# Kernel tuning notes

Measured on AMD Instinct MI355X. Metric: run time of the kernel, lower is better.

Reference implementation:

```python
import jax, jax.numpy as jnp
import numpy as np
from jax import lax

D_MODEL = 1024
N_HEADS = 16
D_STATE = 1024
D_INNER = 1024
D_CONV = 4
CHUNK = 64
BATCH = 2
SEQ = 4096
CONV_DIM = 2 * D_STATE + D_INNER  # 3072
D_IN_PROJ = CONV_DIM + N_HEADS    # 3088


def segsum(a):
    """a: [..., T] -> [..., T, T] segment-sum: out[i,j] = sum_{j<k<=i} a[k], -inf above diag."""
    T = a.shape[-1]
    idx = jnp.arange(T)
    strict = idx[:, None] > idx[None, :]          # i > j
    xx = jnp.where(strict, a[..., :, None], 0.0)  # broadcast a along new last (e) dim
    s = jnp.cumsum(xx, axis=-2)
    incl = idx[:, None] >= idx[None, :]
    return jnp.where(incl, s, -jnp.inf)


def ssd(xv, A, Bm, Cm, l):
    """Mamba-2 SSD chunked scan with max-normalized decays and norm denominator.
    xv:[b,S,h,p] A:[b,S,h] Bm:[b,S,h,n] Cm:[b,S,h,n]"""
    b, S, h, p = xv.shape
    n = Bm.shape[-1]
    c = S // l
    xv = xv.reshape(b, c, l, h, p)
    A = A.reshape(b, c, l, h)
    Bm = Bm.reshape(b, c, l, h, n)
    Cm = Cm.reshape(b, c, l, h, n)
    A = jnp.transpose(A, (0, 3, 1, 2))                  # b h c l
    A_cumsum = jnp.cumsum(A, axis=-1)                   # b h c l
    L_log = segsum(A)                                   # b h c l l
    L = jnp.exp(L_log - jnp.max(L_log, axis=-1, keepdims=True))
    norm_diag = jnp.transpose(L.sum(-1), (0, 2, 3, 1))  # b c l h
    Y_diag = jnp.einsum('bclhn,bcshn,bhcls,bcshp->bclhp', Cm, Bm, L, xv)
    decay_states = A_cumsum[..., -1:] - A_cumsum        # b h c l
    decay_states = jnp.exp(decay_states - jnp.max(decay_states, axis=-1, keepdims=True))
    norm_decay = jnp.transpose(decay_states.sum(-1), (0, 2, 1))  # b c h
    states = jnp.einsum('bclhn,bhcl,bclhp->bchpn', Bm, decay_states, xv)
    norm_decay = jnp.pad(norm_decay, ((0, 0), (1, 0), (0, 0)))
    states = jnp.pad(states, ((0, 0), (1, 0), (0, 0), (0, 0), (0, 0)))
    A_last = jnp.pad(A_cumsum[..., -1], ((0, 0), (0, 0), (1, 0)))  # b h c+1
    decay_chunk = segsum(A_last)                        # b h c+1 c+1
    decay_chunk = jnp.exp(decay_chunk - jnp.max(decay_chunk, axis=-1, keepdims=True))
    norm_decay = jnp.einsum('bhzc,bch->bzh', decay_chunk, norm_decay)[:, :-1]  # b c h
    states = jnp.einsum('bhzc,bchpn->bzhpn', decay_chunk, states)[:, :-1]      # b c h p n
    state_decay_out = jnp.exp(A_cumsum - jnp.max(A_cumsum, axis=-1, keepdims=True))
    norm_off = jnp.einsum('bch,bhcl->bclh', norm_decay, state_decay_out)
    Y_off = jnp.einsum('bclhn,bchpn,bhcl->bclhp', Cm, states, state_decay_out)
    Y = (Y_diag + Y_off).reshape(b, S, h, p)
    norm = (norm_diag + norm_off).reshape(b, S, h)
    return Y / norm[..., None]


def setup_inputs() -> dict:
    key = jax.random.key(0)
    ks = jax.random.split(key, 6)
    x = jax.random.normal(ks[0], (BATCH, SEQ, D_MODEL), dtype=jnp.float32)
    in_proj_w = jax.random.normal(ks[1], (D_IN_PROJ, D_MODEL), dtype=jnp.float32) * 0.02
    conv_w = jax.random.normal(ks[2], (CONV_DIM, 1, D_CONV), dtype=jnp.float32) * 0.3
    conv_b = jnp.zeros((CONV_DIM,), dtype=jnp.float32)
    w_base = jax.random.uniform(ks[3], (N_HEADS,), dtype=jnp.float32, minval=-0.5, maxval=0.5)
    out_proj_w = jax.random.normal(ks[4], (D_MODEL, D_INNER), dtype=jnp.float32) * 0.02
    return {"x": x, "in_proj_w": in_proj_w, "conv_w": conv_w, "conv_b": conv_b,
            "w_base": w_base, "out_proj_w": out_proj_w}


def reference(x, in_proj_w, conv_w, conv_b, w_base, out_proj_w):
    b, S, _ = x.shape  # S divisible by CHUNK -> no padding branch
    xIOw = x @ in_proj_w.T                                  # [b,S,3088]
    xIO, w = xIOw[..., :CONV_DIM], xIOw[..., CONV_DIM:]
    # causal depthwise conv1d (pad d_conv-1 on both sides, keep first S == left pad)
    y = lax.conv_general_dilated(
        jnp.transpose(xIO, (0, 2, 1)), conv_w, window_strides=(1,),
        padding=[(D_CONV - 1, 0)], feature_group_count=CONV_DIM,
        dimension_numbers=('NCH', 'OIH', 'NCH'))
    xIO = jnp.transpose(y + conv_b[None, :, None], (0, 2, 1))  # [b,S,3072]
    xs = xIO[..., :D_STATE].reshape(b, S, N_HEADS, D_STATE // N_HEADS)
    I = xIO[..., D_STATE:2 * D_STATE].reshape(b, S, N_HEADS, D_STATE // N_HEADS)
    O = xIO[..., 2 * D_STATE:].reshape(b, S, N_HEADS, D_INNER // N_HEADS)
    w = w * w_base                                          # [b,S,h]
    out = ssd(O, w, I, xs, CHUNK)                           # [b,S,h,p]
    out = out.reshape(b, S, D_INNER) @ out_proj_w.T
    return out[:, :S]
```

## Files before the change

### kernel.cpp

```cpp
#include <hip/hip_runtime.h>
#include <hip/hip_bf16.h>
#include <math.h>
#include <stdint.h>

#define SEQL 4096
#define NH 16
#define CDIM 3072
#define DPROJ 3088
#define DMODEL 1024

typedef __bf16 nbf16;
typedef __attribute__((ext_vector_type(8))) __bf16 bf16x8;
typedef __attribute__((ext_vector_type(4))) float f32x4;

__device__ inline void store_val(float* p, float v) { *p = v; }
__device__ inline void store_val(nbf16* p, float v) { *p = (nbf16)v; }

__device__ __forceinline__ void gload_lds16(const void* g, void* l) {
  __builtin_amdgcn_global_load_lds(
      (const __attribute__((address_space(1))) void*)g,
      (__attribute__((address_space(3))) void*)l, 16, 0, 0);
}

__device__ __forceinline__ int swz(int row, int col) {
  return row * 64 + (col ^ ((row & 7) << 3));
}

template <typename TOUT>
__global__ __launch_bounds__(512) void gemm_mfma(const nbf16* __restrict__ A,
                                                 const nbf16* __restrict__ B,
                                                 TOUT* __restrict__ C,
                                                 int M, int N, int K) {
  __shared__ __align__(16) nbf16 Alds[256 * 64];
  __shared__ __align__(16) nbf16 Blds[128 * 64];
  int tid = threadIdx.x;
  int lane = tid & 63;
  int w = tid >> 6, wm = w >> 1, wn = w & 1;
  int gx = gridDim.x;
  int nwg = gx * gridDim.y;
  int orig = blockIdx.y * gx + blockIdx.x;
  int wg = (orig & 7) * (nwg >> 3) + (orig >> 3);
  int bm = (wg / gx) * 256, bn = (wg % gx) * 128;
  f32x4 acc[4][4] = {};
  const nbf16* Ag = A + (size_t)bm * K;
  const nbf16* Bg = B + (size_t)bn * K;
  for (int k0 = 0; k0 < K; k0 += 64) {
#pragma unroll
    for (int q = 0; q < 4; ++q) {
      int e = (q * 512 + tid) * 8;
      int row = e >> 6, col = e & 63;
      gload_lds16(Ag + (size_t)row * K + k0 + col, &Alds[e]);
    }
#pragma unroll
    for (int q = 0; q < 2; ++q) {
      int e = (q * 512 + tid) * 8;
      int row = e >> 6, col = e & 63;
      gload_lds16(Bg + (size_t)row * K + k0 + col, &Blds[e]);
    }
    __syncthreads();
#pragma unroll
    for (int kk = 0; kk < 64; kk += 32) {
      bf16x8 af[4], bfr[4];
#pragma unroll
      for (int i = 0; i < 4; ++i) {
        af[i]  = *(const bf16x8*)&Alds[(wm * 64 + i * 16 + (lane & 15)) * 64 + kk + (lane >> 4) * 8];
        bfr[i] = *(const bf16x8*)&Blds[(wn * 64 + i * 16 + (lane & 15)) * 64 + kk + (lane >> 4) * 8];
      }
#pragma unroll
      for (int mi = 0; mi < 4; ++mi)
#pragma unroll
        for (int ni = 0; ni < 4; ++ni)
          acc[mi][ni] = __builtin_amdgcn_mfma_f32_16x16x32_bf16(af[mi], bfr[ni], acc[mi][ni], 0, 0, 0);
    }
    __syncthreads();
  }
#pragma unroll
  for (int mi = 0; mi < 4; ++mi)
#pragma unroll
    for (int ni = 0; ni < 4; ++ni) {
      int colw = bn + wn * 64 + ni * 16 + (lane & 15);
      if (colw >= N) continue;
#pragma unroll
      for (int j = 0; j < 4; ++j) {
        int roww = bm + wm * 64 + mi * 16 + (lane >> 4) * 4 + j;
        store_val(&C[(size_t)roww * N + colw], acc[mi][ni][j]);
      }
    }
}

__global__ __launch_bounds__(256) void cast_bf16(const float* __restrict__ in,
                                                 nbf16* __restrict__ out, long n) {
  long i = ((long)blockIdx.x * 256 + threadIdx.x) * 4;
  if (i >= n) return;
  float4 v = *(const float4*)(in + i);
  out[i] = (nbf16)v.x; out[i + 1] = (nbf16)v.y;
  out[i + 2] = (nbf16)v.z; out[i + 3] = (nbf16)v.w;
}

__global__ __launch_bounds__(256) void cast_pad_w(const float* __restrict__ in,
                                                  nbf16* __restrict__ out) {
  long i = ((long)blockIdx.x * 256 + threadIdx.x) * 4;
  if (i >= (long)3200 * 1024) return;
  int row = (int)(i >> 10);
  if (row < DPROJ) {
    float4 v = *(const float4*)(in + i);
    out[i] = (nbf16)v.x; out[i + 1] = (nbf16)v.y;
    out[i + 2] = (nbf16)v.z; out[i + 3] = (nbf16)v.w;
  } else {
    out[i] = (nbf16)0.f; out[i + 1] = (nbf16)0.f;
    out[i + 2] = (nbf16)0.f; out[i + 3] = (nbf16)0.f;
  }
}

__global__ __launch_bounds__(256) void ssd_intra(
    const nbf16* __restrict__ xw, const float* __restrict__ cw,
    const float* __restrict__ cb, const float* __restrict__ wbase,
    nbf16* __restrict__ Ydg, nbf16* __restrict__ stG,
    float* __restrict__ norm_diag, float* __restrict__ sdo_g,
    float* __restrict__ ndecay, float* __restrict__ Alast) {
  __shared__ __align__(16) nbf16 Craw[68 * 64];
  __shared__ __align__(16) nbf16 Braw[68 * 64];
  __shared__ __align__(16) nbf16 Xraw[68 * 64];
  __shared__ __align__(16) nbf16 BbT[64 * 64];
  __shared__ __align__(16) nbf16 XbT[64 * 64];
  __shared__ float cums_s[64], mincs_s[64], dec_s[64];
  nbf16* Sb = Xraw;

  int tid = threadIdx.x;
  int lane = tid & 63;
  int w = tid >> 6;
  int h = blockIdx.x & 15;
  int c = (blockIdx.x >> 4) & 63;
  int b = blockIdx.x >> 10;

  for (int i = tid; i < 67 * 8; i += 256) {
    int row = i >> 3, n0 = (i & 7) * 8;
    int t = c * 64 - 3 + row;
    bf16x8 vc = {}, vb = {}, vx = {};
    if (t >= 0) {
      const nbf16* r = xw + ((size_t)(b * SEQL + t)) * DPROJ + h * 64 + n0;
      vc = *(const bf16x8*)(r);
      vb = *(const bf16x8*)(r + 1024);
      vx = *(const bf16x8*)(r + 2048);
    }
    int idx = swz(row, n0);
    *(bf16x8*)&Craw[idx] = vc;
    *(bf16x8*)&Braw[idx] = vb;
    *(bf16x8*)&Xraw[idx] = vx;
  }

  if (w == 0) {
    float a = (float)xw[((size_t)(b * SEQL + c * 64 + lane)) * DPROJ + CDIM + h] * wbase[h];
    float cum = a;
#pragma unroll
    for (int d = 1; d < 64; d <<= 1) {
      float t = __shfl_up(cum, d, 64);
      if (lane >= d) cum += t;
    }
    float mn = cum;
#pragma unroll
    for (int d = 1; d < 64; d <<= 1) {
      float t = __shfl_up(mn, d, 64);
      if (lane >= d) mn = fminf(mn, t);
    }
    float mnall = __shfl(mn, 63, 64);
    float mx = cum;
#pragma unroll
    for (int d = 1; d < 64; d <<= 1) mx = fmaxf(mx, __shfl_xor(mx, d, 64));
    float dec = expf(mnall - cum);
    float sdo = expf(cum - mx);
    float nd = dec;
#pragma unroll
    for (int d = 1; d < 64; d <<= 1) nd += __shfl_xor(nd, d, 64);
    cums_s[lane] = cum; mincs_s[lane] = mn; dec_s[lane] = dec;
    sdo_g[(size_t)blockIdx.x * 64 + lane] = sdo;
    if (lane == 0) ndecay[blockIdx.x] = nd;
    if (lane == 63) Alast[((size_t)(b * NH + h)) * 64 + c] = cum;
  }
  __syncthreads();

  float rc[16], rb[16], rx[16];
  {
    int n = tid & 63, base = tid >> 6;
    const float* wcc = cw + (size_t)(h * 64 + n) * 4;
    const float* wcb = wcc + 4096;
    const float* wcx = wcc + 8192;
    float bcc = cb[h * 64 + n], bcb = cb[1024 + h * 64 + n], bcx = cb[2048 + h * 64 + n];
#pragma unroll
    for (int q = 0; q < 16; ++q) {
      int l = base + q * 4;
      float aC = bcc, aB = bcb, aX = bcx;
#pragma unroll
      for (int d = 0; d < 4; ++d) {
        int idx = swz(l + d, n);
        aC = fmaf((float)Craw[idx], wcc[d], aC);
        aB = fmaf((float)Braw[idx], wcb[d], aB);
        aX = fmaf((float)Xraw[idx], wcx[d], aX);
      }
      rc[q] = aC; rb[q] = aB; rx[q] = aX;
    }
  }
  __syncthreads();
  {
    int n = tid & 63, base = tid >> 6;
#pragma unroll
    for (int q = 0; q < 16; ++q) {
      int l = base + q * 4;
      Craw[swz(l, n)] = (nbf16)rc[q];
      Braw[swz(l, n)] = (nbf16)rb[q];
      BbT[swz(n, l)] = (nbf16)rb[q];
      XbT[swz(n, l)] = (nbf16)rx[q];
    }
  }
  __syncthreads();

  {
    f32x4 accS[4] = {};
#pragma unroll
    for (int kk = 0; kk < 64; kk += 32) {
      int arow = w * 16 + (lane & 15);
      int c0 = kk + (lane >> 4) * 8;
      bf16x8 af = *(const bf16x8*)&Craw[swz(arow, c0)];
#pragma unroll
      for (int nb = 0; nb < 4; ++nb) {
        int brow = nb * 16 + (lane & 15);
        bf16x8 bfr = *(const bf16x8*)&Braw[swz(brow, c0)];
        accS[nb] = __builtin_amdgcn_mfma_f32_16x16x32_bf16(af, bfr, accS[nb], 0, 0, 0);
      }
    }
    float rowsum[4] = {0.f, 0.f, 0.f, 0.f};
#pragma unroll
    for (int nb = 0; nb < 4; ++nb) {
      int s = nb * 16 + (lane & 15);
      float cs = cums_s[s];
#pragma unroll
      for (int r = 0; r < 4; ++r) {
        int l = w * 16 + (lane >> 4) * 4 + r;
        float e = (s <= l) ? expf(mincs_s[l] - cs) : 0.f;
        rowsum[r] += e;
        Sb[swz(l, s)] = (nbf16)(accS[nb][r] * e);
      }
    }
#pragma unroll
    for (int r = 0; r < 4; ++r) {
#pragma unroll
      for (int d = 1; d < 16; d <<= 1) rowsum[r] += __shfl_xor(rowsum[r], d, 64);
      if ((lane & 15) == 0) {
        int l = w * 16 + (lane >> 4) * 4 + r;
        norm_diag[(size_t)blockIdx.x * 64 + l] = rowsum[r];
      }
    }
  }
  __syncthreads();

  {
    f32x4 accY[4] = {};
#pragma unroll
    for (int kk = 0; kk < 64; kk += 32) {
      int arow = w * 16 + (lane & 15);
      int c0 = kk + (lane >> 4) * 8;
      bf16x8 af = *(const bf16x8*)&Sb[swz(arow, c0)];
#pragma unroll
      for (int pb = 0; pb < 4; ++pb) {
        int prow = pb * 16 + (lane & 15);
        bf16x8 bfr = *(const bf16x8*)&XbT[swz(prow, c0)];
        accY[pb] = __builtin_amdgcn_mfma_f32_16x16x32_bf16(af, bfr, accY[pb], 0, 0, 0);
      }
    }
    size_t ybase = ((size_t)(b * SEQL + c * 64)) * DMODEL + h * 64;
#pragma unroll
    for (int pb = 0; pb < 4; ++pb) {
      int p = pb * 16 + (lane & 15);
#pragma unroll
      for (int r = 0; r < 4; ++r) {
        int l = w * 16 + (lane >> 4) * 4 + r;
        Ydg[ybase + (size_t)l * DMODEL + p] = (nbf16)accY[pb][r];
      }
    }
  }

  {
    f32x4 accT[4] = {};
#pragma unroll
    for (int kk = 0; kk < 64; kk += 32) {
      int prow = w * 16 + (lane & 15);
      int c0 = kk + (lane >> 4) * 8;
      bf16x8 xf = *(const bf16x8*)&XbT[swz(prow, c0)];
      bf16x8 af;
#pragma unroll
      for (int j = 0; j < 8; ++j) af[j] = (nbf16)((float)xf[j] * dec_s[c0 + j]);
#pragma unroll
      for (int nb = 0; nb < 4; ++nb) {
        int nrow = nb * 16 + (lane & 15);
        bf16x8 bfr = *(const bf16x8*)&BbT[swz(nrow, c0)];
        accT[nb] = __builtin_amdgcn_mfma_f32_16x16x32_bf16(af, bfr, accT[nb], 0, 0, 0);
      }
    }
    size_t sbase = (((size_t)(b * NH + h)) * 64 + c) * 4096;
#pragma unroll
    for (int nb = 0; nb < 4; ++nb) {
      int n = nb * 16 + (lane & 15);
#pragma unroll
      for (int r = 0; r < 4; ++r) {
        int p = w * 16 + (lane >> 4) * 4 + r;
        stG[sbase + p * 64 + n] = (nbf16)accT[nb][r];
      }
    }
  }
}

__global__ __launch_bounds__(256) void ssd_scan(
    const float* __restrict__ Alast, const nbf16* __restrict__ stG,
    const float* __restrict__ ndecay, nbf16* __restrict__ siG,
    float* __restrict__ nd_in) {
  __shared__ __align__(16) nbf16 Msw[64 * 64];
  __shared__ __align__(16) nbf16 StT[256 * 64];
  __shared__ float Qs[66], mzS[64];
  int tid = threadIdx.x, lane = tid & 63, w = tid >> 6;
  int et = blockIdx.x & 15, h = (blockIdx.x >> 4) & 15, b = blockIdx.x >> 8;

  if (w == 0) {
    float a = Alast[((size_t)(b * NH + h)) * 64 + lane];
    float s = a;
#pragma unroll
    for (int d = 1; d < 64; d <<= 1) {
      float t = __shfl_up(s, d, 64);
      if (lane >= d) s += t;
    }
    float Q = __shfl_up(s, 1, 64);
    if (lane == 0) Q = 0.f;
    float m = Q;
#pragma unroll
    for (int d = 1; d < 64; d <<= 1) {
      float t = __shfl_up(m, d, 64);
      if (lane >= d) m = fminf(m, t);
    }
    Qs[lane] = Q; mzS[lane] = m;
    if (lane == 0) { Qs[64] = 0.f; Qs[65] = 0.f; }
  }
  __syncthreads();

#pragma unroll
  for (int k = 0; k < 16; ++k) {
    int i = tid + (k << 8);
    int z = i >> 6, j = i & 63;
    float v = (j < z) ? expf(mzS[z] - Qs[j + 1]) : 0.f;
    Msw[swz(z, j)] = (nbf16)v;
  }
  size_t stbase = ((size_t)(b * NH + h)) * 64 * 4096 + et * 256;
#pragma unroll
  for (int q = 0; q < 8; ++q) {
    int i = tid + (q << 8);
    int cc = i >> 5, oct = i & 31;
    bf16x8 v = *(const bf16x8*)&stG[stbase + (size_t)cc * 4096 + oct * 8];
#pragma unroll
    for (int jj = 0; jj < 8; ++jj) StT[swz(oct * 8 + jj, cc)] = v[jj];
  }
  __syncthreads();

  if (et == 0 && tid < 64) {
    int z = tid;
    float acc = 0.f;
    for (int j = 0; j < z; ++j)
      acc += expf(mzS[z] - Qs[j + 1]) * ndecay[((size_t)(b * 64 + j)) * 16 + h];
    nd_in[((size_t)(b * 64 + z)) * 16 + h] = acc;
  }

  f32x4 acc[4][4] = {};
#pragma unroll
  for (int kk = 0; kk < 64; kk += 32) {
    int c0 = kk + (lane >> 4) * 8;
    bf16x8 af[4], bfr[4];
#pragma unroll
    for (int i = 0; i < 4; ++i) {
      af[i]  = *(const bf16x8*)&Msw[swz(i * 16 + (lane & 15), c0)];
      bfr[i] = *(const bf16x8*)&StT[swz(w * 64 + i * 16 + (lane & 15), c0)];
    }
#pragma unroll
    for (int mi = 0; mi < 4; ++mi)
#pragma unroll
      for (int ni = 0; ni < 4; ++ni)
        acc[mi][ni] = __builtin_amdgcn_mfma_f32_16x16x32_bf16(af[mi], bfr[ni], acc[mi][ni], 0, 0, 0);
  }
  size_t obase = ((size_t)(b * NH + h)) * 64 * 4096 + et * 256;
#pragma unroll
  for (int mi = 0; mi < 4; ++mi)
#pragma unroll
    for (int ni = 0; ni < 4; ++ni) {
      int e = w * 64 + ni * 16 + (lane & 15);
#pragma unroll
      for (int r = 0; r < 4; ++r) {
        int z = mi * 16 + (lane >> 4) * 4 + r;
        siG[obase + (size_t)z * 4096 + e] = (nbf16)acc[mi][ni][r];
      }
    }
}

__global__ __launch_bounds__(256) void ssd_off(
    const nbf16* __restrict__ xw, const float* __restrict__ cw,
    const float* __restrict__ cb, const nbf16* __restrict__ siG,
    const float* __restrict__ norm_diag, const float* __restrict__ sdo_g,
    const float* __restrict__ nd_in, nbf16* __restrict__ Ydg) {
  __shared__ __align__(16) nbf16 Craw[68 * 64];
  __shared__ __align__(16) nbf16 Ssb[64 * 64];
  int tid = threadIdx.x, lane = tid & 63, w = tid >> 6;
  int h = blockIdx.x & 15, c = (blockIdx.x >> 4) & 63, b = blockIdx.x >> 10;

  for (int i = tid; i < 67 * 8; i += 256) {
    int row = i >> 3, n0 = (i & 7) * 8;
    int t = c * 64 - 3 + row;
    bf16x8 v = {};
    if (t >= 0) v = *(const bf16x8*)(xw + ((size_t)(b * SEQL + t)) * DPROJ + h * 64 + n0);
    *(bf16x8*)&Craw[swz(row, n0)] = v;
  }
  {
    size_t sbase = (((size_t)(b * NH + h)) * 64 + c) * 4096;
    for (int i = tid; i < 512; i += 256) {
      int p = i >> 3, n0 = (i & 7) * 8;
      bf16x8 v = *(const bf16x8*)&siG[sbase + p * 64 + n0];
      *(bf16x8*)&Ssb[swz(p, n0)] = v;
    }
  }
  __syncthreads();

  float rc[16];
  {
    int n = tid & 63, base = tid >> 6;
    const float* wcc = cw + (size_t)(h * 64 + n) * 4;
    float bcc = cb[h * 64 + n];
#pragma unroll
    for (int q = 0; q < 16; ++q) {
      int l = base + q * 4;
      float aC = bcc;
#pragma unroll
      for (int d = 0; d < 4; ++d) aC = fmaf((float)Craw[swz(l + d, n)], wcc[d], aC);
      rc[q] = aC;
    }
  }
  __syncthreads();
  {
    int n = tid & 63, base = tid >> 6;
#pragma unroll
    for (int q = 0; q < 16; ++q) Craw[swz(base + q * 4, n)] = (nbf16)rc[q];
  }
  __syncthreads();

  f32x4 accO[4] = {};
#pragma unroll
  for (int kk = 0; kk < 64; kk += 32) {
    int arow = w * 16 + (lane & 15);
    int c0 = kk + (lane >> 4) * 8;
    bf16x8 af = *(const bf16x8*)&Craw[swz(arow, c0)];
#pragma unroll
    for (int pb = 0; pb < 4; ++pb) {
      int prow = pb * 16 + (lane & 15);
      bf16x8 bfr = *(const bf16x8*)&Ssb[swz(prow, c0)];
      accO[pb] = __builtin_amdgcn_mfma_f32_16x16x32_bf16(af, bfr, accO[pb], 0, 0, 0);
    }
  }
  float ndin = nd_in[blockIdx.x];
  size_t ybase = ((size_t)(b * SEQL + c * 64)) * DMODEL + h * 64;
#pragma unroll
  for (int r = 0; r < 4; ++r) {
    int l = w * 16 + (lane >> 4) * 4 + r;
    float sd = sdo_g[(size_t)blockIdx.x * 64 + l];
    float nrm = norm_diag[(size_t)blockIdx.x * 64 + l] + ndin * sd;
#pragma unroll
    for (int pb = 0; pb < 4; ++pb) {
      int p = pb * 16 + (lane & 15);
      size_t yi = ybase + (size_t)l * DMODEL + p;
      Ydg[yi] = (nbf16)(((float)Ydg[yi] + accO[pb][r] * sd) / nrm);
    }
  }
}

extern "C" void kernel_launch(void* const* d_in, const int* in_sizes, int n_in,
                              void* d_out, int out_size, void* d_ws, size_t ws_size,
                              hipStream_t stream) {
  const float* x          = (const float*)d_in[0];
  const float* in_proj_w  = (const float*)d_in[1];
  const float* conv_w     = (const float*)d_in[2];
  const float* conv_b     = (const float*)d_in[3];
  const float* w_base     = (const float*)d_in[4];
  const float* out_proj_w = (const float*)d_in[5];
  float* out = (float*)d_out;

  char* ws = (char*)d_ws;
  size_t off = 0;
  auto alloc = [&](size_t bytes) {
    void* p = ws + off;
    off += (bytes + 255) & ~(size_t)255;
    return p;
  };
  const size_t BT = (size_t)2 * SEQL;
  nbf16* xIOw = (nbf16*)alloc(BT * DPROJ * 2);
  nbf16* xbf  = (nbf16*)alloc(BT * DMODEL * 2);
  nbf16* wibf = (nbf16*)alloc((size_t)3200 * 1024 * 2);
  nbf16* wobf = (nbf16*)alloc((size_t)1024 * 1024 * 2);
  nbf16* stG  = (nbf16*)alloc((size_t)2048 * 4096 * 2);
  nbf16* siG  = (nbf16*)alloc((size_t)2048 * 4096 * 2);
  float* norm_diag = (float*)alloc((size_t)2048 * 64 * 4);
  float* sdo   = (float*)alloc((size_t)2048 * 64 * 4);
  float* ndec  = (float*)alloc((size_t)2048 * 4);
  float* Alast = (float*)alloc((size_t)2048 * 4);
  float* nd_in = (float*)alloc((size_t)2048 * 4);
  nbf16* Ydg = xbf;

  cast_bf16<<<(int)(BT * DMODEL / 4 / 256), 256, 0, stream>>>(x, xbf, BT * DMODEL);
  cast_pad_w<<<3200 * 1024 / 4 / 256, 256, 0, stream>>>(in_proj_w, wibf);
  cast_bf16<<<DMODEL * DMODEL / 4 / 256, 256, 0, stream>>>(out_proj_w, wobf, (long)DMODEL * DMODEL);
  gemm_mfma<nbf16><<<dim3(25, BT / 256), 512, 0, stream>>>(
      xbf, wibf, xIOw, (int)BT, DPROJ, DMODEL);
  ssd_intra<<<2048, 256, 0, stream>>>(xIOw, conv_w, conv_b, w_base,
                                      Ydg, stG, norm_diag, sdo, ndec, Alast);
  ssd_scan<<<512, 256, 0, stream>>>(Alast, stG, ndec, siG, nd_in);
  ssd_off<<<2048, 256, 0, stream>>>(xIOw, conv_w, conv_b, siG,
                                    norm_diag, sdo, nd_in, Ydg);
  gemm_mfma<float><<<dim3(DMODEL / 128, BT / 256), 512, 0, stream>>>(
      Ydg, wobf, out, (int)BT, DMODEL, DMODEL);
}
```

Baseline: 301.9 us.

## Double-buffer GEMM LDS tiles with XOR swizzle and smaller 128x128 blocks

Rewrites the MFMA GEMM to use two LDS buffers so the next K-tile's global-to-LDS loads are issued while the current tile is computed. Loads are placed with an XOR swizzle to cut LDS bank conflicts on fragment reads. The block tile shrinks from 256x128 with 512 threads to 128x128 with 256 threads, giving more workgroups. This trades higher LDS footprint per block and less reuse per tile for load/compute overlap and better occupancy.

```diff
diff --git a/kernel.cpp b/kernel.cpp
--- a/kernel.cpp
+++ b/kernel.cpp
@@ -27,12 +27,12 @@
 }
 
 template <typename TOUT>
-__global__ __launch_bounds__(512) void gemm_mfma(const nbf16* __restrict__ A,
+__global__ __launch_bounds__(256) void gemm_mfma(const nbf16* __restrict__ A,
                                                  const nbf16* __restrict__ B,
                                                  TOUT* __restrict__ C,
                                                  int M, int N, int K) {
-  __shared__ __align__(16) nbf16 Alds[256 * 64];
-  __shared__ __align__(16) nbf16 Blds[128 * 64];
+  __shared__ __align__(16) nbf16 Alds[2][128 * 64];
+  __shared__ __align__(16) nbf16 Blds[2][128 * 64];
   int tid = threadIdx.x;
   int lane = tid & 63;
   int w = tid >> 6, wm = w >> 1, wn = w & 1;
@@ -40,31 +40,32 @@
   int nwg = gx * gridDim.y;
   int orig = blockIdx.y * gx + blockIdx.x;
   int wg = (orig & 7) * (nwg >> 3) + (orig >> 3);
-  int bm = (wg / gx) * 256, bn = (wg % gx) * 128;
-  f32x4 acc[4][4] = {};
+  int bm = (wg / gx) * 128, bn = (wg % gx) * 128;
   const nbf16* Ag = A + (size_t)bm * K;
   const nbf16* Bg = B + (size_t)bn * K;
-  for (int k0 = 0; k0 < K; k0 += 64) {
+  f32x4 acc[4][4] = {};
+  const int nt = K >> 6;
+
+  auto STAGE = [&](int buf, int k0) {
 #pragma unroll
     for (int q = 0; q < 4; ++q) {
-      int e = (q * 512 + tid) * 8;
-      int row = e >> 6, col = e & 63;
-      gload_lds16(Ag + (size_t)row * K + k0 + col, &Alds[e]);
-    }
-#pragma unroll
-    for (int q = 0; q < 2; ++q) {
-      int e = (q * 512 + tid) * 8;
-      int row = e >> 6, col = e & 63;
-      gload_lds16(Bg + (size_t)row * K + k0 + col, &Blds[e]);
-    }
-    __syncthreads();
+      int e = (q * 256 + tid) * 8;
+      int row = e >> 6;
+      int cs = (e >> 3) & 7;
+      int sc = (cs ^ (row & 7)) << 3;
+      gload_lds16(Ag + (size_t)row * K + k0 + sc, &Alds[buf][e]);
+      gload_lds16(Bg + (size_t)row * K + k0 + sc, &Blds[buf][e]);
+    }
+  };
+  auto COMPUTE = [&](int buf) {
 #pragma unroll
     for (int kk = 0; kk < 64; kk += 32) {
       bf16x8 af[4], bfr[4];
+      int col = kk + (lane >> 4) * 8;
 #pragma unroll
       for (int i = 0; i < 4; ++i) {
-        af[i]  = *(const bf16x8*)&Alds[(wm * 64 + i * 16 + (lane & 15)) * 64 + kk + (lane >> 4) * 8];
-        bfr[i] = *(const bf16x8*)&Blds[(wn * 64 + i * 16 + (lane & 15)) * 64 + kk + (lane >> 4) * 8];
+        af[i]  = *(const bf16x8*)&Alds[buf][swz(wm * 64 + i * 16 + (lane & 15), col)];
+        bfr[i] = *(const bf16x8*)&Blds[buf][swz(wn * 64 + i * 16 + (lane & 15), col)];
       }
 #pragma unroll
       for (int mi = 0; mi < 4; ++mi)
@@ -72,8 +73,20 @@
         for (int ni = 0; ni < 4; ++ni)
           acc[mi][ni] = __builtin_amdgcn_mfma_f32_16x16x32_bf16(af[mi], bfr[ni], acc[mi][ni], 0, 0, 0);
     }
-    __syncthreads();
-  }
+  };
+
+  STAGE(0, 0);
+  asm volatile("s_waitcnt vmcnt(0)" ::: "memory");
+  __builtin_amdgcn_s_barrier();
+  for (int t = 0; t < nt - 1; ++t) {
+    int cur = t & 1;
+    STAGE(cur ^ 1, (t + 1) << 6);
+    COMPUTE(cur);
+    asm volatile("s_waitcnt vmcnt(0)" ::: "memory");
+    __builtin_amdgcn_s_barrier();
+  }
+  COMPUTE((nt - 1) & 1);
+
 #pragma unroll
   for (int mi = 0; mi < 4; ++mi)
 #pragma unroll
@@ -509,13 +522,13 @@
   cast_bf16<<<(int)(BT * DMODEL / 4 / 256), 256, 0, stream>>>(x, xbf, BT * DMODEL);
   cast_pad_w<<<3200 * 1024 / 4 / 256, 256, 0, stream>>>(in_proj_w, wibf);
   cast_bf16<<<DMODEL * DMODEL / 4 / 256, 256, 0, stream>>>(out_proj_w, wobf, (long)DMODEL * DMODEL);
-  gemm_mfma<nbf16><<<dim3(25, BT / 256), 512, 0, stream>>>(
+  gemm_mfma<nbf16><<<dim3(25, BT / 128), 256, 0, stream>>>(
       xbf, wibf, xIOw, (int)BT, DPROJ, DMODEL);
   ssd_intra<<<2048, 256, 0, stream>>>(xIOw, conv_w, conv_b, w_base,
                                       Ydg, stG, norm_diag, sdo, ndec, Alast);
   ssd_scan<<<512, 256, 0, stream>>>(Alast, stG, ndec, siG, nd_in);
   ssd_off<<<2048, 256, 0, stream>>>(xIOw, conv_w, conv_b, siG,
                                     norm_diag, sdo, nd_in, Ydg);
-  gemm_mfma<float><<<dim3(DMODEL / 128, BT / 256), 512, 0, stream>>>(
+  gemm_mfma<float><<<dim3(DMODEL / 128, BT / 128), 256, 0, stream>>>(
       Ydg, wobf, out, (int)BT, DMODEL, DMODEL);
 }
```

Result: faster. 291.0 us (-3.6%).
